# Performance work log

Measured on AMD Instinct MI355X. Metric: run time of the kernel, lower is better.

Reference implementation:

```python
import jax, jax.numpy as jnp
import numpy as np

N_NODES = 100000
N_EDGES = 3200000
IN_DIM, HID_DIM, OUT_DIM = 128, 8, 1


def _graph_conv(x, src, dst, W, b, n_nodes):
    """DGL GraphConv, norm='both', weight applied before aggregation
    (valid since in_feats > out_feats for both layers).
    out = D_in^{-1/2} * scatter_sum_dst( (D_out^{-1/2} * x W)[src] ) + b
    """
    ones_e = jnp.ones((src.shape[0],), dtype=x.dtype)
    deg_out = jax.ops.segment_sum(ones_e, src, num_segments=n_nodes)
    deg_in = jax.ops.segment_sum(ones_e, dst, num_segments=n_nodes)
    norm_out = jnp.clip(deg_out, 1.0, None) ** -0.5  # [N]
    norm_in = jnp.clip(deg_in, 1.0, None) ** -0.5    # [N]
    h = (x * norm_out[:, None]) @ W                   # [N, out_dim] small GEMM first
    msg = h[src]                                      # [E, out_dim] gather
    agg = jax.ops.segment_sum(msg, dst, num_segments=n_nodes)  # [N, out_dim] scatter
    return agg * norm_in[:, None] + b


def setup_inputs() -> dict:
    key = jax.random.key(0)
    k0, k1, k2, k3, k4, k5, k6 = jax.random.split(key, 7)
    x = jax.random.normal(k0, (N_NODES, IN_DIM), dtype=jnp.float32)
    src = jax.random.randint(k1, (N_EDGES,), 0, N_NODES, dtype=jnp.int64)
    dst = jax.random.randint(k2, (N_EDGES,), 0, N_NODES, dtype=jnp.int64)
    # Glorot-uniform weights as in DGL GraphConv reset_parameters
    lim1 = float(np.sqrt(6.0 / (IN_DIM + HID_DIM)))
    lim2 = float(np.sqrt(6.0 / (HID_DIM + OUT_DIM)))
    W1 = jax.random.uniform(k3, (IN_DIM, HID_DIM), minval=-lim1, maxval=lim1, dtype=jnp.float32)
    b1 = jnp.zeros((HID_DIM,), dtype=jnp.float32)
    W2 = jax.random.uniform(k4, (HID_DIM, OUT_DIM), minval=-lim2, maxval=lim2, dtype=jnp.float32)
    b2 = jnp.zeros((OUT_DIM,), dtype=jnp.float32)
    return {"x": x, "src": src, "dst": dst, "W1": W1, "b1": b1, "W2": W2, "b2": b2}


def reference(x, src, dst, W1, b1, W2, b2):
    h = _graph_conv(x, src, dst, W1, b1, N_NODES)   # conv1: 128 -> 8
    h = jax.nn.relu(h)
    out = _graph_conv(h, src, dst, W2, b2, N_NODES)  # conv2: 8 -> 1
    return out
```

## Files before the change

kernel.cpp:

```cpp
#include <hip/hip_runtime.h>
#include <hip/hip_bf16.h>
#include <hip/hip_fp16.h>

#define IN_DIM 128
#define HID 8
#define TW 256
#define MAXT 512
#define CCH 256

__global__ __launch_bounds__(1024) void pass1AB_kernel(const int* __restrict__ src, const int* __restrict__ dst,
        int* __restrict__ cntS, int* __restrict__ cntD, int E, int RT, int chunk) {
    __shared__ int cs[MAXT], cd[MAXT];
    int t = threadIdx.x, c = blockIdx.x;
    for (int i = t; i < RT; i += 1024) { cs[i] = 0; cd[i] = 0; }
    __syncthreads();
    int lo = c * chunk, hi = min(lo + chunk, E);
    if (lo < hi) {
        const int4* s4 = reinterpret_cast<const int4*>(src);
        const int4* d4 = reinterpret_cast<const int4*>(dst);
        int q0 = lo >> 2, q1 = hi >> 2;
        for (int q = q0 + t; q < q1; q += 1024) {
            int4 s = s4[q], d = d4[q];
            atomicAdd(&cs[s.x >> 8], 1); atomicAdd(&cs[s.y >> 8], 1);
            atomicAdd(&cs[s.z >> 8], 1); atomicAdd(&cs[s.w >> 8], 1);
            atomicAdd(&cd[d.x >> 8], 1); atomicAdd(&cd[d.y >> 8], 1);
            atomicAdd(&cd[d.z >> 8], 1); atomicAdd(&cd[d.w >> 8], 1);
        }
        for (int i = (q1 << 2) + t; i < hi; i += 1024) {
            atomicAdd(&cs[src[i] >> 8], 1);
            atomicAdd(&cd[dst[i] >> 8], 1);
        }
    }
    __syncthreads();
    for (int i = t; i < RT; i += 1024) {
        cntS[(size_t)c * RT + i] = cs[i];
        cntD[(size_t)c * RT + i] = cd[i];
    }
}

__global__ __launch_bounds__(256) void scan1_kernel(int* __restrict__ cntS, int* __restrict__ cntD,
        int* __restrict__ totS, int* __restrict__ totD, int RT) {
    int r = blockIdx.x;
    int* cnt = blockIdx.y ? cntD : cntS;
    int* tot = blockIdx.y ? totD : totS;
    __shared__ int sh[256];
    int t = threadIdx.x;
    int e = cnt[(size_t)t * RT + r];
    sh[t] = e;
    __syncthreads();
    for (int off = 1; off < 256; off <<= 1) {
        int v = (t >= off) ? sh[t - off] : 0;
        __syncthreads();
        sh[t] += v;
        __syncthreads();
    }
    cnt[(size_t)t * RT + r] = sh[t] - e;
    if (t == 255) tot[r] = sh[255];
}

__global__ __launch_bounds__(256) void scan2_kernel(const int* __restrict__ totS, const int* __restrict__ totD,
        int* __restrict__ baseS, int* __restrict__ baseD, int RT) {
    const int* tot = blockIdx.x ? totD : totS;
    int* base = blockIdx.x ? baseD : baseS;
    __shared__ int sh[256];
    int t = threadIdx.x;
    int K = (RT + 255) / 256;
    int vals[4];
    int s = 0;
    for (int k = 0; k < K; ++k) {
        int i = t * K + k;
        int v = (i < RT) ? tot[i] : 0;
        vals[k] = v; s += v;
    }
    sh[t] = s;
    __syncthreads();
    for (int off = 1; off < 256; off <<= 1) {
        int v = (t >= off) ? sh[t - off] : 0;
        __syncthreads();
        sh[t] += v;
        __syncthreads();
    }
    int exc = sh[t] - s;
    for (int k = 0; k < K; ++k) {
        int i = t * K + k;
        if (i < RT) base[i] = exc;
        exc += vals[k];
    }
    if (t == 255) base[RT] = sh[255];
}

__global__ __launch_bounds__(1024) void scatterAB_kernel(const int* __restrict__ src, const int* __restrict__ dst,
        const int* __restrict__ cntS, const int* __restrict__ cntD,
        const int* __restrict__ baseS, const int* __restrict__ baseD,
        unsigned char* __restrict__ bucket_s, unsigned int* __restrict__ bucketT,
        int E, int RT, int chunk) {
    __shared__ int os[MAXT], od[MAXT];
    int t = threadIdx.x;
    int c = ((blockIdx.x & 7) << 5) | (blockIdx.x >> 3);
    for (int i = t; i < RT; i += 1024) {
        os[i] = baseS[i] + cntS[(size_t)c * RT + i];
        od[i] = baseD[i] + cntD[(size_t)c * RT + i];
    }
    __syncthreads();
    int lo = c * chunk, hi = min(lo + chunk, E);
    if (lo >= hi) return;
    const int4* s4 = reinterpret_cast<const int4*>(src);
    const int4* d4 = reinterpret_cast<const int4*>(dst);
    int q0 = lo >> 2, q1 = hi >> 2;
    for (int q = q0 + t; q < q1; q += 1024) {
        int4 s = s4[q], d = d4[q];
        int p;
        p = atomicAdd(&os[s.x >> 8], 1); bucket_s[p] = (unsigned char)(s.x & 255);
        p = atomicAdd(&os[s.y >> 8], 1); bucket_s[p] = (unsigned char)(s.y & 255);
        p = atomicAdd(&os[s.z >> 8], 1); bucket_s[p] = (unsigned char)(s.z & 255);
        p = atomicAdd(&os[s.w >> 8], 1); bucket_s[p] = (unsigned char)(s.w & 255);
        p = atomicAdd(&od[d.x >> 8], 1); bucketT[p] = ((unsigned)s.x << 8) | (unsigned)(d.x & 255);
        p = atomicAdd(&od[d.y >> 8], 1); bucketT[p] = ((unsigned)s.y << 8) | (unsigned)(d.y & 255);
        p = atomicAdd(&od[d.z >> 8], 1); bucketT[p] = ((unsigned)s.z << 8) | (unsigned)(d.z & 255);
        p = atomicAdd(&od[d.w >> 8], 1); bucketT[p] = ((unsigned)s.w << 8) | (unsigned)(d.w & 255);
    }
    for (int i = (q1 << 2) + t; i < hi; i += 1024) {
        int s = src[i], d = dst[i];
        int p = atomicAdd(&os[s >> 8], 1);
        bucket_s[p] = (unsigned char)(s & 255);
        p = atomicAdd(&od[d >> 8], 1);
        bucketT[p] = ((unsigned)s << 8) | (unsigned)(d & 255);
    }
}

__global__ __launch_bounds__(512) void passC_kernel(const unsigned int* __restrict__ bucketT,
        const int* __restrict__ baseD, unsigned int* __restrict__ bucketG,
        int* __restrict__ row_ptr, int E, int RT) {
    __shared__ int cnt[TW];
    __shared__ int scn[TW];
    __shared__ int start[TW];
    int r = blockIdx.x, t = threadIdx.x;
    if (t < TW) cnt[t] = 0;
    __syncthreads();
    int lo = baseD[r], hi = baseD[r + 1];
    for (int i = lo + t; i < hi; i += 512) atomicAdd(&cnt[bucketT[i] & 255u], 1);
    __syncthreads();
    if (t < TW) scn[t] = cnt[t];
    __syncthreads();
    for (int off = 1; off < TW; off <<= 1) {
        int v = 0;
        if (t < TW && t >= off) v = scn[t - off];
        __syncthreads();
        if (t < TW) scn[t] += v;
        __syncthreads();
    }
    if (t < TW) {
        int ex = scn[t] - cnt[t];
        start[t] = ex;
        row_ptr[r * TW + t] = lo + ex;
    }
    if (r == 0 && t == 0) row_ptr[RT * TW] = E;
    __syncthreads();
    for (int i = lo + t; i < hi; i += 512) {
        unsigned v = bucketT[i];
        int p = atomicAdd(&start[v & 255u], 1);
        bucketG[lo + p] = v >> 8;
    }
}

__global__ __launch_bounds__(256) void conv1deg_kernel(
        const unsigned char* __restrict__ bucket_s, const int* __restrict__ baseS,
        const float* __restrict__ x, const float* __restrict__ W1,
        float* __restrict__ deg_out, uint4* __restrict__ h4, int N) {
    __shared__ float wt[HID * 132];
    __shared__ int cnt[TW];
    __shared__ float nrmS[TW];
    int r = blockIdx.x, t = threadIdx.x;
    for (int i = t; i < IN_DIM * HID; i += 256) {
        int k = i >> 3, j = i & 7;
        wt[j * 132 + k] = W1[i];
    }
    cnt[t] = 0;
    __syncthreads();
    int lo = baseS[r], hi = baseS[r + 1];
    int a0 = min((lo + 3) & ~3, hi), a1 = max(hi & ~3, a0);
    for (int i = lo + t; i < a0; i += 256) atomicAdd(&cnt[bucket_s[i]], 1);
    const unsigned* w4 = reinterpret_cast<const unsigned*>(bucket_s);
    for (int q = (a0 >> 2) + t; q < (a1 >> 2); q += 256) {
        unsigned w = w4[q];
        atomicAdd(&cnt[w & 255], 1);
        atomicAdd(&cnt[(w >> 8) & 255], 1);
        atomicAdd(&cnt[(w >> 16) & 255], 1);
        atomicAdd(&cnt[w >> 24], 1);
    }
    for (int i = a1 + t; i < hi; i += 256) atomicAdd(&cnt[bucket_s[i]], 1);
    __syncthreads();
    {
        int node = r * TW + t;
        if (node < N) deg_out[node] = (float)cnt[t];
        nrmS[t] = rsqrtf(fmaxf((float)cnt[t], 1.0f));
    }
    __syncthreads();
    int grp = t >> 3, lane = t & 7;
    #pragma unroll
    for (int sweep = 0; sweep < 8; ++sweep) {
        int nl = sweep * 32 + grp;
        int node = r * TW + nl;
        if (node < N) {
            const float4* xp = reinterpret_cast<const float4*>(x + (size_t)node * IN_DIM);
            float4 xv[4];
            #pragma unroll
            for (int m = 0; m < 4; ++m) xv[m] = xp[lane + m * 8];
            float acc[HID];
            #pragma unroll
            for (int j = 0; j < HID; ++j) acc[j] = 0.f;
            #pragma unroll
            for (int j = 0; j < HID; ++j) {
                #pragma unroll
                for (int m = 0; m < 4; ++m) {
                    float4 wv = *reinterpret_cast<const float4*>(&wt[j * 132 + lane * 4 + m * 32]);
                    acc[j] += xv[m].x * wv.x + xv[m].y * wv.y + xv[m].z * wv.z + xv[m].w * wv.w;
                }
            }
            #pragma unroll
            for (int off = 1; off < 8; off <<= 1) {
                #pragma unroll
                for (int j = 0; j < HID; ++j) acc[j] += __shfl_xor(acc[j], off, 64);
            }
            if (lane == 0) {
                float nrm = nrmS[nl];
                __half2 p0 = __floats2half2_rn(acc[0] * nrm, acc[1] * nrm);
                __half2 p1 = __floats2half2_rn(acc[2] * nrm, acc[3] * nrm);
                __half2 p2 = __floats2half2_rn(acc[4] * nrm, acc[5] * nrm);
                __half2 p3 = __floats2half2_rn(acc[6] * nrm, acc[7] * nrm);
                uint4 o;
                o.x = *reinterpret_cast<unsigned*>(&p0);
                o.y = *reinterpret_cast<unsigned*>(&p1);
                o.z = *reinterpret_cast<unsigned*>(&p2);
                o.w = *reinterpret_cast<unsigned*>(&p3);
                h4[node] = o;
            }
        }
    }
}

__device__ __forceinline__ void accAdd(float* acc, uint4 g) {
    __half2 q0 = *reinterpret_cast<__half2*>(&g.x);
    __half2 q1 = *reinterpret_cast<__half2*>(&g.y);
    __half2 q2 = *reinterpret_cast<__half2*>(&g.z);
    __half2 q3 = *reinterpret_cast<__half2*>(&g.w);
    float2 f0 = __half22float2(q0), f1 = __half22float2(q1);
    float2 f2 = __half22float2(q2), f3 = __half22float2(q3);
    acc[0] += f0.x; acc[1] += f0.y;
    acc[2] += f1.x; acc[3] += f1.y;
    acc[4] += f2.x; acc[5] += f2.y;
    acc[6] += f3.x; acc[7] += f3.y;
}

__global__ __launch_bounds__(256) void agg1G4_kernel(const unsigned int* __restrict__ bucketG,
        const int* __restrict__ row_ptr, const uint4* __restrict__ h4,
        const float* __restrict__ deg_out, const float* __restrict__ b1, const float* __restrict__ W2,
        float* __restrict__ h2, int N) {
    int tid = blockIdx.x * 256 + threadIdx.x;
    int node = tid >> 2, sub = tid & 3;
    int s0 = row_ptr[node], s1 = row_ptr[node + 1];
    float acc[HID];
    #pragma unroll
    for (int j = 0; j < HID; ++j) acc[j] = 0.f;
    for (int e = s0 + sub; e < s1; e += 4) accAdd(acc, h4[bucketG[e]]);
    #pragma unroll
    for (int off = 1; off < 4; off <<= 1) {
        #pragma unroll
        for (int j = 0; j < HID; ++j) acc[j] += __shfl_xor(acc[j], off, 64);
    }
    if (sub == 0 && node < N) {
        float din = (float)(s1 - s0);
        float nin = rsqrtf(fmaxf(din, 1.f));
        float nout = rsqrtf(fmaxf(deg_out[node], 1.f));
        float dot = 0.f;
        #pragma unroll
        for (int j = 0; j < HID; ++j) {
            float y = fmaxf(acc[j] * nin + b1[j], 0.f);
            dot += y * W2[j];
        }
        h2[node] = dot * nout;
    }
}

__global__ __launch_bounds__(256) void agg2G4_kernel(const unsigned int* __restrict__ bucketG,
        const int* __restrict__ row_ptr, const float* __restrict__ h2,
        const float* __restrict__ b2, float* __restrict__ out, int N) {
    int tid = blockIdx.x * 256 + threadIdx.x;
    int node = tid >> 2, sub = tid & 3;
    int s0 = row_ptr[node], s1 = row_ptr[node + 1];
    float a = 0.f;
    for (int e = s0 + sub; e < s1; e += 4) a += h2[bucketG[e]];
    a += __shfl_xor(a, 1, 64);
    a += __shfl_xor(a, 2, 64);
    if (sub == 0 && node < N) {
        float nin = rsqrtf(fmaxf((float)(s1 - s0), 1.f));
        out[node] = a * nin + b2[0];
    }
}

extern "C" void kernel_launch(void* const* d_in, const int* in_sizes, int n_in,
                              void* d_out, int out_size, void* d_ws, size_t ws_size,
                              hipStream_t stream) {
    const float* x  = (const float*)d_in[0];
    const int* src  = (const int*)d_in[1];
    const int* dst  = (const int*)d_in[2];
    const float* W1 = (const float*)d_in[3];
    const float* b1 = (const float*)d_in[4];
    const float* W2 = (const float*)d_in[5];
    const float* b2 = (const float*)d_in[6];
    float* out = (float*)d_out;

    const int N  = out_size;
    const int E  = in_sizes[1];
    const int RT = (N + TW - 1) / TW;
    const int chunk = (((E + CCH - 1) / CCH) + 3) & ~3;

    float* ws      = (float*)d_ws;
    float* deg_out = ws;
    float* h2      = deg_out + N;
    int*   cntS    = (int*)(h2 + N);
    int*   cntD    = cntS + (size_t)CCH * RT;
    int*   totS    = cntD + (size_t)CCH * RT;
    int*   baseS   = totS + RT;
    int*   totD    = baseS + RT + 1;
    int*   baseD   = totD + RT;
    int*   row_ptr = baseD + RT + 1;
    unsigned int* bucketT = (unsigned int*)(row_ptr + (size_t)RT * TW + 1);
    unsigned int* bucketG = bucketT + E;
    uint4* h4 = (uint4*)(((uintptr_t)(bucketG + E) + 15) & ~(uintptr_t)15);
    unsigned char* bucket_s = (unsigned char*)(h4 + N);

    pass1AB_kernel<<<CCH, 1024, 0, stream>>>(src, dst, cntS, cntD, E, RT, chunk);
    scan1_kernel<<<dim3(RT, 2), 256, 0, stream>>>(cntS, cntD, totS, totD, RT);
    scan2_kernel<<<2, 256, 0, stream>>>(totS, totD, baseS, baseD, RT);
    scatterAB_kernel<<<CCH, 1024, 0, stream>>>(src, dst, cntS, cntD, baseS, baseD,
                                               bucket_s, bucketT, E, RT, chunk);
    passC_kernel<<<RT, 512, 0, stream>>>(bucketT, baseD, bucketG, row_ptr, E, RT);
    conv1deg_kernel<<<RT, 256, 0, stream>>>(bucket_s, baseS, x, W1, deg_out, h4, N);
    agg1G4_kernel<<<RT * 4, 256, 0, stream>>>(bucketG, row_ptr, h4, deg_out, b1, W2, h2, N);
    agg2G4_kernel<<<RT * 4, 256, 0, stream>>>(bucketG, row_ptr, h2, b2, out, N);
}
```

Measured before the change: 130.0 us.

## Fuse destination-bucket sort with layer-1 aggregation using LDS-resident sorted indices

Merges the per-bucket counting sort (passC) with the first-layer gather-aggregate into one kernel per 256-node bucket. The sorted source indices are kept in shared memory (up to CAP entries), so the layer-1 aggregation reads them from LDS rather than re-reading bucketG from global memory. bucketG and row_ptr are still written out for the second layer. The cost is one launch per bucket with only 512 threads and about 48KB of LDS, which lowers occupancy and parallelism compared with the separate agg1 kernel that used four times as many blocks.

New measurement: 113.9 us. -12.4%, faster.

```diff
diff --git a/kernel.cpp b/kernel.cpp
--- a/kernel.cpp
+++ b/kernel.cpp
@@ -7,6 +7,7 @@
 #define TW 256
 #define MAXT 512
 #define CCH 256
+#define CAP 12288
 
 __global__ __launch_bounds__(1024) void pass1AB_kernel(const int* __restrict__ src, const int* __restrict__ dst,
         int* __restrict__ cntS, int* __restrict__ cntD, int E, int RT, int chunk) {
@@ -125,41 +126,6 @@
         bucket_s[p] = (unsigned char)(s & 255);
         p = atomicAdd(&od[d >> 8], 1);
         bucketT[p] = ((unsigned)s << 8) | (unsigned)(d & 255);
-    }
-}
-
-__global__ __launch_bounds__(512) void passC_kernel(const unsigned int* __restrict__ bucketT,
-        const int* __restrict__ baseD, unsigned int* __restrict__ bucketG,
-        int* __restrict__ row_ptr, int E, int RT) {
-    __shared__ int cnt[TW];
-    __shared__ int scn[TW];
-    __shared__ int start[TW];
-    int r = blockIdx.x, t = threadIdx.x;
-    if (t < TW) cnt[t] = 0;
-    __syncthreads();
-    int lo = baseD[r], hi = baseD[r + 1];
-    for (int i = lo + t; i < hi; i += 512) atomicAdd(&cnt[bucketT[i] & 255u], 1);
-    __syncthreads();
-    if (t < TW) scn[t] = cnt[t];
-    __syncthreads();
-    for (int off = 1; off < TW; off <<= 1) {
-        int v = 0;
-        if (t < TW && t >= off) v = scn[t - off];
-        __syncthreads();
-        if (t < TW) scn[t] += v;
-        __syncthreads();
-    }
-    if (t < TW) {
-        int ex = scn[t] - cnt[t];
-        start[t] = ex;
-        row_ptr[r * TW + t] = lo + ex;
-    }
-    if (r == 0 && t == 0) row_ptr[RT * TW] = E;
-    __syncthreads();
-    for (int i = lo + t; i < hi; i += 512) {
-        unsigned v = bucketT[i];
-        int p = atomicAdd(&start[v & 255u], 1);
-        bucketG[lo + p] = v >> 8;
     }
 }
 
@@ -252,33 +218,85 @@
     acc[6] += f3.x; acc[7] += f3.y;
 }
 
-__global__ __launch_bounds__(256) void agg1G4_kernel(const unsigned int* __restrict__ bucketG,
-        const int* __restrict__ row_ptr, const uint4* __restrict__ h4,
-        const float* __restrict__ deg_out, const float* __restrict__ b1, const float* __restrict__ W2,
-        float* __restrict__ h2, int N) {
-    int tid = blockIdx.x * 256 + threadIdx.x;
-    int node = tid >> 2, sub = tid & 3;
-    int s0 = row_ptr[node], s1 = row_ptr[node + 1];
-    float acc[HID];
+__global__ __launch_bounds__(512) void sortagg1_kernel(
+        const unsigned int* __restrict__ bucketT, const int* __restrict__ baseD,
+        unsigned int* __restrict__ bucketG, int* __restrict__ row_ptr,
+        const uint4* __restrict__ h4, const float* __restrict__ deg_out,
+        const float* __restrict__ b1, const float* __restrict__ W2,
+        float* __restrict__ h2, int E, int RT, int N) {
+    __shared__ unsigned sorted[CAP];
+    __shared__ int cnt[TW], scn[TW], start[TW];
+    __shared__ float b1s[HID], w2s[HID];
+    int r = blockIdx.x, t = threadIdx.x;
+    if (t < TW) cnt[t] = 0;
+    if (t < HID) { b1s[t] = b1[t]; w2s[t] = W2[t]; }
+    __syncthreads();
+    int lo = baseD[r], hi = baseD[r + 1], len = hi - lo;
+    for (int i = lo + t; i < hi; i += 512) atomicAdd(&cnt[bucketT[i] & 255u], 1);
+    __syncthreads();
+    if (t < TW) scn[t] = cnt[t];
+    __syncthreads();
+    for (int off = 1; off < TW; off <<= 1) {
+        int v = 0;
+        if (t < TW && t >= off) v = scn[t - off];
+        __syncthreads();
+        if (t < TW) scn[t] += v;
+        __syncthreads();
+    }
+    if (t < TW) {
+        start[t] = scn[t] - cnt[t];
+        row_ptr[r * TW + t] = lo + scn[t] - cnt[t];
+    }
+    if (r == 0 && t == 0) row_ptr[RT * TW] = E;
+    __syncthreads();
+    bool fits = (len <= CAP);
+    if (fits) {
+        for (int i = lo + t; i < hi; i += 512) {
+            unsigned v = bucketT[i];
+            int p = atomicAdd(&start[v & 255u], 1);
+            sorted[p] = v >> 8;
+        }
+        __syncthreads();
+        for (int i = t; i < len; i += 512) bucketG[lo + i] = sorted[i];
+    } else {
+        for (int i = lo + t; i < hi; i += 512) {
+            unsigned v = bucketT[i];
+            int p = atomicAdd(&start[v & 255u], 1);
+            bucketG[lo + p] = v >> 8;
+        }
+        __syncthreads();
+    }
     #pragma unroll
-    for (int j = 0; j < HID; ++j) acc[j] = 0.f;
-    for (int e = s0 + sub; e < s1; e += 4) accAdd(acc, h4[bucketG[e]]);
-    #pragma unroll
-    for (int off = 1; off < 4; off <<= 1) {
+    for (int half = 0; half < 2; ++half) {
+        int nl = (t >> 2) + half * 128;
+        int sub = t & 3;
+        int node = r * TW + nl;
+        int end = scn[nl], beg = end - cnt[nl];
+        float acc[HID];
         #pragma unroll
-        for (int j = 0; j < HID; ++j) acc[j] += __shfl_xor(acc[j], off, 64);
-    }
-    if (sub == 0 && node < N) {
-        float din = (float)(s1 - s0);
-        float nin = rsqrtf(fmaxf(din, 1.f));
-        float nout = rsqrtf(fmaxf(deg_out[node], 1.f));
-        float dot = 0.f;
+        for (int j = 0; j < HID; ++j) acc[j] = 0.f;
+        if (fits) {
+            for (int e = beg + sub; e < end; e += 4) accAdd(acc, h4[sorted[e]]);
+        } else {
+            for (int e = beg + sub; e < end; e += 4) accAdd(acc, h4[bucketG[lo + e]]);
+        }
         #pragma unroll
-        for (int j = 0; j < HID; ++j) {
-            float y = fmaxf(acc[j] * nin + b1[j], 0.f);
-            dot += y * W2[j];
-        }
-        h2[node] = dot * nout;
+        for (int off = 1; off < 4; off <<= 1) {
+            #pragma unroll
+            for (int j = 0; j < HID; ++j) acc[j] += __shfl_xor(acc[j], off, 64);
+        }
+        if (sub == 0 && node < N) {
+            float din = (float)(end - beg);
+            float nin = rsqrtf(fmaxf(din, 1.f));
+            float nout = rsqrtf(fmaxf(deg_out[node], 1.f));
+            float dot = 0.f;
+            #pragma unroll
+            for (int j = 0; j < HID; ++j) {
+                float y = fmaxf(acc[j] * nin + b1s[j], 0.f);
+                dot += y * w2s[j];
+            }
+            h2[node] = dot * nout;
+        }
     }
 }
 
@@ -335,8 +353,8 @@
     scan2_kernel<<<2, 256, 0, stream>>>(totS, totD, baseS, baseD, RT);
     scatterAB_kernel<<<CCH, 1024, 0, stream>>>(src, dst, cntS, cntD, baseS, baseD,
                                                bucket_s, bucketT, E, RT, chunk);
-    passC_kernel<<<RT, 512, 0, stream>>>(bucketT, baseD, bucketG, row_ptr, E, RT);
     conv1deg_kernel<<<RT, 256, 0, stream>>>(bucket_s, baseS, x, W1, deg_out, h4, N);
-    agg1G4_kernel<<<RT * 4, 256, 0, stream>>>(bucketG, row_ptr, h4, deg_out, b1, W2, h2, N);
+    sortagg1_kernel<<<RT, 512, 0, stream>>>(bucketT, baseD, bucketG, row_ptr,
+                                            h4, deg_out, b1, W2, h2, E, RT, N);
     agg2G4_kernel<<<RT * 4, 256, 0, stream>>>(bucketG, row_ptr, h2, b2, out, N);
 }
```
